# Kernel tuning notes

Measured on AMD Instinct MI355X. Metric: run time of the kernel, lower is better.

Reference implementation:

```python
import jax, jax.numpy as jnp
import numpy as np

DMODEL = 2048
HEADS = 16
DHEAD = DMODEL // HEADS  # 128


def setup_inputs() -> dict:
    key = jax.random.key(0)
    ks = jax.random.split(key, 9)
    s = 0.02
    x = jax.random.normal(ks[0], (4, 2048, DMODEL), dtype=jnp.float32)
    Wq = jax.random.normal(ks[1], (DMODEL, DMODEL), dtype=jnp.float32) * s
    bq = jax.random.normal(ks[2], (DMODEL,), dtype=jnp.float32) * s
    Wk = jax.random.normal(ks[3], (DMODEL, DMODEL), dtype=jnp.float32) * s
    bk = jax.random.normal(ks[4], (DMODEL,), dtype=jnp.float32) * s
    Wv = jax.random.normal(ks[5], (DMODEL, DMODEL), dtype=jnp.float32) * s
    bv = jax.random.normal(ks[6], (DMODEL,), dtype=jnp.float32) * s
    Wo = jax.random.normal(ks[7], (DMODEL, DMODEL), dtype=jnp.float32) * s
    bo = jax.random.normal(ks[8], (DMODEL,), dtype=jnp.float32) * s
    return {"x": x, "Wq": Wq, "bq": bq, "Wk": Wk, "bk": bk, "Wv": Wv, "bv": bv, "Wo": Wo, "bo": bo}


def reference(x, Wq, bq, Wk, bk, Wv, bv, Wo, bo):
    b, l, _ = x.shape
    # projections: [b, l, dmodel] -> [b, l, heads, dhead]
    q = (x @ Wq + bq).reshape(b, l, HEADS, DHEAD)
    k = (x @ Wk + bk).reshape(b, l, HEADS, DHEAD)
    v = (x @ Wv + bv).reshape(b, l, HEADS, DHEAD)
    # NOTE: source applies 1/sqrt(dhead) twice -> total scale 1/dhead (faithful)
    a = jnp.einsum('blhd,bLhd->bhlL', q, k) * (1.0 / DHEAD)
    a = jax.nn.softmax(a, axis=-1)
    prefinal = jnp.einsum('bhlL,bLhd->blhd', a, v)
    out = prefinal.reshape(b, l, HEADS * DHEAD) @ Wo + bo
    return out
```

## Files before the change

kernel.cpp:

```cpp
#include <hip/hip_runtime.h>

#define DMODEL 2048
#define SEQ    2048
#define BATCH  4
#define HEADS  16
#define DHEAD  128

typedef __attribute__((ext_vector_type(8))) short short8;
typedef __attribute__((ext_vector_type(4))) float f32x4;
typedef __attribute__((ext_vector_type(16))) float f32x16;

__device__ __forceinline__ unsigned short f2bf(float f) {
  union { float f; unsigned u; } v; v.f = f;
  unsigned r = v.u + 0x7FFFu + ((v.u >> 16) & 1u);
  return (unsigned short)(r >> 16);
}

__global__ __launch_bounds__(256) void cvt_f32_bf16(const float* __restrict__ in,
                                                    unsigned short* __restrict__ out,
                                                    int n4) {
  int i = blockIdx.x * 256 + threadIdx.x;
  if (i >= n4) return;
  float4 v = ((const float4*)in)[i];
  ushort4 o;
  o.x = f2bf(v.x); o.y = f2bf(v.y); o.z = f2bf(v.z); o.w = f2bf(v.w);
  ((ushort4*)out)[i] = o;
}

__global__ __launch_bounds__(256) void transpose_cvt4(const float* __restrict__ w0,
                                                      const float* __restrict__ w1,
                                                      const float* __restrict__ w2,
                                                      const float* __restrict__ w3,
                                                      unsigned short* __restrict__ o0,
                                                      unsigned short* __restrict__ o1,
                                                      unsigned short* __restrict__ o2,
                                                      unsigned short* __restrict__ o3) {
  __shared__ float tile[32][33];
  const int z = blockIdx.z;
  const float* in = (z == 0) ? w0 : (z == 1) ? w1 : (z == 2) ? w2 : w3;
  unsigned short* out = (z == 0) ? o0 : (z == 1) ? o1 : (z == 2) ? o2 : o3;
  const int tx = threadIdx.x, ty = threadIdx.y;
  const int x = blockIdx.x * 32 + tx;
  const int y0 = blockIdx.y * 32;
#pragma unroll
  for (int j = 0; j < 32; j += 8)
    tile[ty + j][tx] = in[(size_t)(y0 + ty + j) * DMODEL + x];
  __syncthreads();
  const int xo = blockIdx.y * 32 + tx;
  const int yo0 = blockIdx.x * 32;
#pragma unroll
  for (int j = 0; j < 32; j += 8)
    out[(size_t)(yo0 + ty + j) * DMODEL + xo] = f2bf(tile[tx][ty + j]);
}

__global__ __launch_bounds__(256) void transpose_v(const unsigned short* __restrict__ in,
                                                   unsigned short* __restrict__ out) {
  __shared__ unsigned short t[32][33];
  const int tx = threadIdx.x, ty = threadIdx.y;
  const int bid = blockIdx.x;
  const int lb = bid & 63;
  const int db = (bid >> 6) & 3;
  const int h  = (bid >> 8) & 15;
  const int b  = bid >> 12;
#pragma unroll
  for (int j = 0; j < 32; j += 8)
    t[ty + j][tx] = in[(size_t)(b * SEQ + lb * 32 + ty + j) * DMODEL + h * DHEAD + db * 32 + tx];
  __syncthreads();
  const size_t ob = ((size_t)(b * HEADS + h) * DHEAD + db * 32) * SEQ + lb * 32;
#pragma unroll
  for (int j = 0; j < 32; j += 8)
    out[ob + (size_t)(ty + j) * SEQ + tx] = t[tx][ty + j];
}

template <typename OUT_T, int NTN>
__global__ __launch_bounds__(512, 2) void gemm3(const unsigned short* __restrict__ A,
                                                const unsigned short* __restrict__ Bt,
                                                const float* __restrict__ b0,
                                                const float* __restrict__ b1,
                                                const float* __restrict__ b2,
                                                OUT_T* __restrict__ C) {
  __shared__ unsigned short As[2][256 * 32];
  __shared__ unsigned short Bs[2][256 * 32];

  const int tid = threadIdx.x;
  const int l = tid & 63, w = tid >> 6;
  const int wr = w >> 2, wc = w & 3;

  const int bid = blockIdx.x;
  int tm, tn;
  if constexpr (NTN == 24) {
    const int xcd = bid & 7;
    const int idx = bid >> 3;
    const int r = xcd >> 1, c = xcd & 1;
    const int mt = idx >> 4;
    const int i = idx & 15;
    const int mrow = mt & 1, mcol = mt >> 1;
    tm = r * 8 + mrow * 4 + (i & 3);
    tn = c * 12 + mcol * 4 + (i >> 2);
  } else {
    const int q8 = (32 * NTN) >> 3;
    const int swz = (bid & 7) * q8 + (bid >> 3);
    tn = swz % NTN;
    tm = swz / NTN;
  }

  const int srow = tid >> 2;
  const int schunk = (tid & 3) ^ ((tid >> 3) & 3);
  const unsigned short* Ag0 = A + (size_t)(tm * 256 + srow) * DMODEL + schunk * 8;
  const unsigned short* Ag1 = Ag0 + (size_t)128 * DMODEL;
  const unsigned short* Bg0 = Bt + (size_t)(tn * 256 + srow) * DMODEL + schunk * 8;
  const unsigned short* Bg1 = Bg0 + (size_t)128 * DMODEL;

#define GLL(src, dst) __builtin_amdgcn_global_load_lds( \
    (const __attribute__((address_space(1))) void*)(src), \
    (__attribute__((address_space(3))) void*)(dst), 16, 0, 0)

#define STAGE(bf, kt) do { \
    GLL(Ag0 + (kt) * 32, &As[bf][0 * 4096 + w * 512]); \
    GLL(Ag1 + (kt) * 32, &As[bf][1 * 4096 + w * 512]); \
    GLL(Bg0 + (kt) * 32, &Bs[bf][0 * 4096 + w * 512]); \
    GLL(Bg1 + (kt) * 32, &Bs[bf][1 * 4096 + w * 512]); \
  } while (0)

  f32x4 acc[8][4] = {};
  const int rchunk = ((l >> 4) ^ (((l & 15) >> 1) & 3)) * 8;

  STAGE(0, 0);
  int buf = 0;
  for (int t = 0; t < 64; ++t) {
    __builtin_amdgcn_s_barrier();
    __builtin_amdgcn_sched_barrier(0);
    if (t < 63) {
      STAGE(buf ^ 1, t + 1);
      __builtin_amdgcn_sched_barrier(0);
      asm volatile("s_waitcnt vmcnt(4)" ::: "memory");
    } else {
      asm volatile("s_waitcnt vmcnt(0)" ::: "memory");
    }
    __builtin_amdgcn_sched_barrier(0);
    __builtin_amdgcn_s_barrier();
    __builtin_amdgcn_sched_barrier(0);

    {
      const unsigned short* Asb = &As[buf][0];
      const unsigned short* Bsb = &Bs[buf][0];
      short8 bfr[4];
#pragma unroll
      for (int n = 0; n < 4; ++n) {
        const int row = wc * 64 + n * 16 + (l & 15);
        bfr[n] = *(const short8*)&Bsb[row * 32 + rchunk];
      }
      __builtin_amdgcn_s_setprio(1);
#pragma unroll
      for (int m = 0; m < 8; ++m) {
        const int row = wr * 128 + m * 16 + (l & 15);
        short8 af = *(const short8*)&Asb[row * 32 + rchunk];
#pragma unroll
        for (int n = 0; n < 4; ++n)
          acc[m][n] = __builtin_amdgcn_mfma_f32_16x16x32_bf16(af, bfr[n], acc[m][n], 0, 0, 0);
      }
      __builtin_amdgcn_s_setprio(0);
    }
    buf ^= 1;
  }
#undef STAGE
#undef GLL

  const int bsel = tn >> 3;
  const float* bp = (bsel == 0) ? b0 : ((bsel == 1) ? b1 : b2);
  OUT_T* Cb = C + (size_t)bsel * ((size_t)8192 * DMODEL);
  const int row0 = tm * 256 + wr * 128 + ((l >> 4) * 4);
  const int lc0 = (tn & 7) * 256 + wc * 64 + (l & 15);
#pragma unroll
  for (int n = 0; n < 4; ++n) {
    float bv = bp[lc0 + n * 16];
#pragma unroll
    for (int m = 0; m < 8; ++m) {
#pragma unroll
      for (int r = 0; r < 4; ++r) {
        float v = acc[m][n][r] + bv;
        size_t idx = (size_t)(row0 + m * 16 + r) * DMODEL + (lc0 + n * 16);
        if constexpr (sizeof(OUT_T) == 2) ((unsigned short*)Cb)[idx] = f2bf(v);
        else                              ((float*)Cb)[idx] = v;
      }
    }
  }
}

__global__ __launch_bounds__(256) void attn(const unsigned short* __restrict__ Q,
                                            const unsigned short* __restrict__ K,
                                            const unsigned short* __restrict__ V,
                                            unsigned short* __restrict__ O) {
  __shared__ unsigned short Ks[32 * 136];
  __shared__ unsigned short Vt[128 * 40];
  __shared__ unsigned short Ps[4][16 * 40];

  const int tid = threadIdx.x;
  const int l = tid & 63, w = tid >> 6;
  const int bh = blockIdx.x >> 5, qb = blockIdx.x & 31;
  const int b = bh >> 4, h = bh & 15;
  const size_t base = ((size_t)b * SEQ) * DMODEL + (size_t)h * DHEAD;

  const unsigned short* Qp = Q + base + (size_t)(qb * 64 + w * 16) * DMODEL;
  short8 qf[4];
#pragma unroll
  for (int dc = 0; dc < 4; ++dc)
    qf[dc] = *(const short8*)(Qp + (size_t)(l & 15) * DMODEL + dc * 32 + (l >> 4) * 8);

  f32x4 acc[8] = {};
  float sum[4] = {0.f, 0.f, 0.f, 0.f};

  const int skv = tid >> 3;
  const int sc = (tid & 7) * 16;
  const unsigned short* Kg = K + base + (size_t)skv * DMODEL + sc;
  const unsigned short* Vg = V + base + (size_t)skv * DMODEL + sc;

  const float cexp = 1.4426950408889634f / 128.0f;

  for (int kv0 = 0; kv0 < SEQ; kv0 += 32) {
    __syncthreads();
    short8 ka = *(const short8*)(Kg + (size_t)kv0 * DMODEL);
    short8 kb = *(const short8*)(Kg + (size_t)kv0 * DMODEL + 8);
    *(short8*)&Ks[skv * 136 + sc] = ka;
    *(short8*)&Ks[skv * 136 + sc + 8] = kb;
    short8 va = *(const short8*)(Vg + (size_t)kv0 * DMODEL);
    short8 vb = *(const short8*)(Vg + (size_t)kv0 * DMODEL + 8);
#pragma unroll
    for (int j = 0; j < 8; ++j) {
      Vt[(sc + j) * 40 + skv]     = (unsigned short)va[j];
      Vt[(sc + 8 + j) * 40 + skv] = (unsigned short)vb[j];
    }
    __syncthreads();

    f32x4 s[2];
#pragma unroll
    for (int nh = 0; nh < 2; ++nh) {
      f32x4 t = {};
#pragma unroll
      for (int dc = 0; dc < 4; ++dc) {
        short8 kf = *(const short8*)&Ks[(nh * 16 + (l & 15)) * 136 + dc * 32 + (l >> 4) * 8];
        t = __builtin_amdgcn_mfma_f32_16x16x32_bf16(qf[dc], kf, t, 0, 0, 0);
      }
      s[nh] = t;
    }

#pragma unroll
    for (int nh = 0; nh < 2; ++nh) {
#pragma unroll
      for (int r = 0; r < 4; ++r) {
        float p = exp2f(s[nh][r] * cexp);
        sum[r] += p;
        Ps[w][((l >> 4) * 4 + r) * 40 + (l & 15) + nh * 16] = f2bf(p);
      }
    }

    short8 pf = *(const short8*)&Ps[w][(l & 15) * 40 + (l >> 4) * 8];
#pragma unroll
    for (int db = 0; db < 8; ++db) {
      short8 vf = *(const short8*)&Vt[(db * 16 + (l & 15)) * 40 + (l >> 4) * 8];
      acc[db] = __builtin_amdgcn_mfma_f32_16x16x32_bf16(pf, vf, acc[db], 0, 0, 0);
    }
  }

  float inv[4];
#pragma unroll
  for (int r = 0; r < 4; ++r) {
    float s = sum[r];
    s += __shfl_xor(s, 1);
    s += __shfl_xor(s, 2);
    s += __shfl_xor(s, 4);
    s += __shfl_xor(s, 8);
    inv[r] = 1.0f / s;
  }
  unsigned short* Op = O + base + (size_t)(qb * 64 + w * 16) * DMODEL;
#pragma unroll
  for (int db = 0; db < 8; ++db)
#pragma unroll
    for (int r = 0; r < 4; ++r)
      Op[(size_t)((l >> 4) * 4 + r) * DMODEL + db * 16 + (l & 15)] = f2bf(acc[db][r] * inv[r]);
}

__global__ __launch_bounds__(256, 2) void attn6(const unsigned short* __restrict__ Q,
                                                const unsigned short* __restrict__ K,
                                                const unsigned short* __restrict__ VT,
                                                unsigned short* __restrict__ O) {
  __shared__ unsigned short Ks[2][64 * 128];
  __shared__ unsigned short Vs[2][128 * 64];

  const int tid = threadIdx.x;
  const int l = tid & 63, w = tid >> 6;
  const int x32 = l & 31, h = l >> 5;

  const int bid = blockIdx.x;
  const int swz = (bid & 7) * 64 + (bid >> 3);
  const int bh = swz >> 3, qb = swz & 7;
  const int b = bh >> 4, hh = bh & 15;
  const size_t base = ((size_t)b * SEQ) * DMODEL + (size_t)hh * DHEAD;
  const unsigned short* VTb = VT + (size_t)bh * DHEAD * SEQ;

  const unsigned short* Qp = Q + base + (size_t)(qb * 256 + w * 64) * DMODEL;
  short8 qfA[8], qfB[8];
#pragma unroll
  for (int dc = 0; dc < 8; ++dc) {
    qfA[dc] = *(const short8*)(Qp + (size_t)x32 * DMODEL + dc * 16 + h * 8);
    qfB[dc] = *(const short8*)(Qp + (size_t)(x32 + 32) * DMODEL + dc * 16 + h * 8);
  }

  const unsigned short* Kg0 = K + base + (size_t)(w * 16 + (l >> 4)) * DMODEL + (((l & 15) ^ (l >> 4)) * 8);
  const unsigned short* Kg1 = K + base + (size_t)(w * 16 + (l >> 4)) * DMODEL + (((l & 15) ^ ((l >> 4) + 4)) * 8);
  const unsigned short* Vg0 = VTb + (size_t)(w * 32 + (l >> 3)) * SEQ + (((l & 7) ^ (l >> 3)) * 8);

  unsigned short* KsD = &Ks[0][0];
  unsigned short* VsD = &Vs[0][0];

#define GLL(src, dst) __builtin_amdgcn_global_load_lds( \
    (const __attribute__((address_space(1))) void*)(src), \
    (__attribute__((address_space(3))) void*)(dst), 16, 0, 0)

#define STAGE(bf, kv0) do { \
    GLL(Kg0 + (size_t)(kv0) * DMODEL,        KsD + (bf) * 8192 + w * 2048 + 0 * 512); \
    GLL(Kg1 + (size_t)((kv0) + 4) * DMODEL,  KsD + (bf) * 8192 + w * 2048 + 1 * 512); \
    GLL(Kg0 + (size_t)((kv0) + 8) * DMODEL,  KsD + (bf) * 8192 + w * 2048 + 2 * 512); \
    GLL(Kg1 + (size_t)((kv0) + 12) * DMODEL, KsD + (bf) * 8192 + w * 2048 + 3 * 512); \
    GLL(Vg0 + (size_t)0 * SEQ + (kv0),       VsD + (bf) * 8192 + w * 2048 + 0 * 512); \
    GLL(Vg0 + (size_t)8 * SEQ + (kv0),       VsD + (bf) * 8192 + w * 2048 + 1 * 512); \
    GLL(Vg0 + (size_t)16 * SEQ + (kv0),      VsD + (bf) * 8192 + w * 2048 + 2 * 512); \
    GLL(Vg0 + (size_t)24 * SEQ + (kv0),      VsD + (bf) * 8192 + w * 2048 + 3 * 512); \
  } while (0)

  f32x16 acc0[4] = {}, acc1[4] = {};
  float sum0 = 0.f, sum1 = 0.f;
  const float cexp = 1.4426950408889634f / 128.0f;

#define COMPUTE_SUB(bf, s) do { \
    const unsigned short* Kb_ = &Ks[bf][(s) * 32 * 128]; \
    const unsigned short* Vb_ = &Vs[bf][0]; \
    f32x16 sa0 = {}, sa1 = {}; \
    __builtin_amdgcn_s_setprio(1); \
    _Pragma("unroll") \
    for (int dc = 0; dc < 8; ++dc) { \
      short8 kf = *(const short8*)&Kb_[x32 * 128 + (((dc * 2 + h) ^ (x32 & 7)) * 8)]; \
      sa0 = __builtin_amdgcn_mfma_f32_32x32x16_bf16(kf, qfA[dc], sa0, 0, 0, 0); \
      sa1 = __builtin_amdgcn_mfma_f32_32x32x16_bf16(kf, qfB[dc], sa1, 0, 0, 0); \
    } \
    __builtin_amdgcn_s_setprio(0); \
    union { unsigned u[4]; short8 s8; } pf0A, pf1A, pf0B, pf1B; \
    { \
      float p[16]; \
      _Pragma("unroll") \
      for (int r = 0; r < 16; ++r) { p[r] = __builtin_amdgcn_exp2f(sa0[r] * cexp); sum0 += p[r]; } \
      unsigned pk0[4], pk1[4]; \
      _Pragma("unroll") \
      for (int blk = 0; blk < 4; ++blk) { \
        asm("v_cvt_pk_bf16_f32 %0, %1, %2" : "=v"(pk0[blk]) : "v"(p[blk * 4 + 0]), "v"(p[blk * 4 + 1])); \
        asm("v_cvt_pk_bf16_f32 %0, %1, %2" : "=v"(pk1[blk]) : "v"(p[blk * 4 + 2]), "v"(p[blk * 4 + 3])); \
      } \
      unsigned a0 = pk0[0], a1 = pk0[1], b0 = pk1[0], b1 = pk1[1]; \
      asm("v_permlane32_swap_b32 %0, %1" : "+v"(a0), "+v"(a1)); \
      asm("v_permlane32_swap_b32 %0, %1" : "+v"(b0), "+v"(b1)); \
      pf0A.u[0] = a0; pf0A.u[1] = b0; pf0A.u[2] = a1; pf0A.u[3] = b1; \
      unsigned c0 = pk0[2], c1 = pk0[3], d0 = pk1[2], d1 = pk1[3]; \
      asm("v_permlane32_swap_b32 %0, %1" : "+v"(c0), "+v"(c1)); \
      asm("v_permlane32_swap_b32 %0, %1" : "+v"(d0), "+v"(d1)); \
      pf1A.u[0] = c0; pf1A.u[1] = d0; pf1A.u[2] = c1; pf1A.u[3] = d1; \
    } \
    { \
      float p[16]; \
      _Pragma("unroll") \
      for (int r = 0; r < 16; ++r) { p[r] = __builtin_amdgcn_exp2f(sa1[r] * cexp); sum1 += p[r]; } \
      unsigned pk0[4], pk1[4]; \
      _Pragma("unroll") \
      for (int blk = 0; blk < 4; ++blk) { \
        asm("v_cvt_pk_bf16_f32 %0, %1, %2" : "=v"(pk0[blk]) : "v"(p[blk * 4 + 0]), "v"(p[blk * 4 + 1])); \
        asm("v_cvt_pk_bf16_f32 %0, %1, %2" : "=v"(pk1[blk]) : "v"(p[blk * 4 + 2]), "v"(p[blk * 4 + 3])); \
      } \
      unsigned a0 = pk0[0], a1 = pk0[1], b0 = pk1[0], b1 = pk1[1]; \
      asm("v_permlane32_swap_b32 %0, %1" : "+v"(a0), "+v"(a1)); \
      asm("v_permlane32_swap_b32 %0, %1" : "+v"(b0), "+v"(b1)); \
      pf0B.u[0] = a0; pf0B.u[1] = b0; pf0B.u[2] = a1; pf0B.u[3] = b1; \
      unsigned c0 = pk0[2], c1 = pk0[3], d0 = pk1[2], d1 = pk1[3]; \
      asm("v_permlane32_swap_b32 %0, %1" : "+v"(c0), "+v"(c1)); \
      asm("v_permlane32_swap_b32 %0, %1" : "+v"(d0), "+v"(d1)); \
      pf1B.u[0] = c0; pf1B.u[1] = d0; pf1B.u[2] = c1; pf1B.u[3] = d1; \
    } \
    __builtin_amdgcn_s_setprio(1); \
    _Pragma("unroll") \
    for (int db = 0; db < 4; ++db) { \
      const int row = db * 32 + x32; \
      short8 vf0 = *(const short8*)&Vb_[row * 64 + ((((s) * 4 + 0 + h) ^ (row & 7)) * 8)]; \
      short8 vf1 = *(const short8*)&Vb_[row * 64 + ((((s) * 4 + 2 + h) ^ (row & 7)) * 8)]; \
      acc0[db] = __builtin_amdgcn_mfma_f32_32x32x16_bf16(pf0A.s8, vf0, acc0[db], 0, 0, 0); \
      acc1[db] = __builtin_amdgcn_mfma_f32_32x32x16_bf16(pf0B.s8, vf0, acc1[db], 0, 0, 0); \
      acc0[db] = __builtin_amdgcn_mfma_f32_32x32x16_bf16(pf1A.s8, vf1, acc0[db], 0, 0, 0); \
      acc1[db] = __builtin_amdgcn_mfma_f32_32x32x16_bf16(pf1B.s8, vf1, acc1[db], 0, 0, 0); \
    } \
    __builtin_amdgcn_s_setprio(0); \
  } while (0)

  STAGE(0, 0);
  int buf = 0;
  for (int t = 0; t < 32; ++t) {
    __builtin_amdgcn_s_barrier();
    __builtin_amdgcn_sched_barrier(0);
    if (t < 31) {
      STAGE(buf ^ 1, (t + 1) * 64);
      __builtin_amdgcn_sched_barrier(0);
      asm volatile("s_waitcnt vmcnt(8)" ::: "memory");
    } else {
      asm volatile("s_waitcnt vmcnt(0)" ::: "memory");
    }
    __builtin_amdgcn_sched_barrier(0);
    __builtin_amdgcn_s_barrier();
    __builtin_amdgcn_sched_barrier(0);
    COMPUTE_SUB(buf, 0);
    COMPUTE_SUB(buf, 1);
    buf ^= 1;
  }
#undef COMPUTE_SUB
#undef STAGE
#undef GLL

  sum0 += __shfl_xor(sum0, 32);
  sum1 += __shfl_xor(sum1, 32);
  float inv0 = 1.0f / sum0;
  float inv1 = 1.0f / sum1;
  float invq0[16], invq1[16];
#pragma unroll
  for (int r = 0; r < 16; ++r) {
    const int crow = (r & 3) + 8 * (r >> 2) + 4 * h;
    invq0[r] = __shfl(inv0, crow);
    invq1[r] = __shfl(inv1, crow);
  }

  unsigned short* Op = O + base + (size_t)(qb * 256 + w * 64) * DMODEL;
#pragma unroll
  for (int db = 0; db < 4; ++db)
#pragma unroll
    for (int r = 0; r < 16; ++r) {
      const int crow = (r & 3) + 8 * (r >> 2) + 4 * h;
      Op[(size_t)crow * DMODEL + db * 32 + x32] = f2bf(acc0[db][r] * invq0[r]);
      Op[(size_t)(crow + 32) * DMODEL + db * 32 + x32] = f2bf(acc1[db][r] * invq1[r]);
    }
}

extern "C" void kernel_launch(void* const* d_in, const int* in_sizes, int n_in,
                              void* d_out, int out_size, void* d_ws, size_t ws_size,
                              hipStream_t stream) {
  const float* x  = (const float*)d_in[0];
  const float* Wq = (const float*)d_in[1];
  const float* bq = (const float*)d_in[2];
  const float* Wk = (const float*)d_in[3];
  const float* bk = (const float*)d_in[4];
  const float* Wv = (const float*)d_in[5];
  const float* bv = (const float*)d_in[6];
  const float* Wo = (const float*)d_in[7];
  const float* bo = (const float*)d_in[8];

  char* ws = (char*)d_ws;
  unsigned short* xb  = (unsigned short*)ws;
  unsigned short* WqT = (unsigned short*)(ws + 33554432);
  unsigned short* WkT = (unsigned short*)(ws + 41943040);
  unsigned short* WvT = (unsigned short*)(ws + 50331648);
  unsigned short* WoT = (unsigned short*)(ws + 58720256);
  unsigned short* Qb  = (unsigned short*)(ws + 67108864);
  unsigned short* Kb  = (unsigned short*)(ws + 100663296);
  unsigned short* Vb  = (unsigned short*)(ws + 134217728);
  unsigned short* VTg = (unsigned short*)(ws + 167772160);
  unsigned short* Pf  = xb;

  const bool vt_ok = (ws_size >= (size_t)201326592);

  cvt_f32_bf16<<<16384, 256, 0, stream>>>(x, xb, (BATCH * SEQ * DMODEL) / 4);

  transpose_cvt4<<<dim3(64, 64, 4), dim3(32, 8), 0, stream>>>(Wq, Wk, Wv, Wo, WqT, WkT, WvT, WoT);

  gemm3<unsigned short, 24><<<768, 512, 0, stream>>>(xb, WqT, bq, bk, bv, Qb);

  if (vt_ok) {
    transpose_v<<<16384, dim3(32, 8), 0, stream>>>(Vb, VTg);
    attn6<<<512, 256, 0, stream>>>(Qb, Kb, VTg, Pf);
  } else {
    attn<<<2048, 256, 0, stream>>>(Qb, Kb, Vb, Pf);
  }

  gemm3<float, 8><<<256, 512, 0, stream>>>(Pf, WoT, bo, bo, bo, (float*)d_out);
}
```

Baseline: 580.8 us.

## Restructure projection GEMM to 4 waves with 128x128 warp tiles and K=64 stages

Replaces the 8-wave, 256x256-tile GEMM (64x128 per-wave sub-tiles, K-step 32) with a 4-wave version where each wave computes a 128x128 sub-tile and each LDS stage covers K=64 with an XOR swizzle over 8 chunks. This raises MFMA work per LDS fragment load and halves the number of barrier-synchronised iterations. In exchange the 256 accumulator registers per lane push the kernel to one block per CU, and LDS use doubles to 128 KB, which cuts occupancy and latency hiding.

```diff
diff --git a/kernel.cpp b/kernel.cpp
--- a/kernel.cpp
+++ b/kernel.cpp
@@ -73,18 +73,18 @@
 }
 
 template <typename OUT_T, int NTN>
-__global__ __launch_bounds__(512, 2) void gemm3(const unsigned short* __restrict__ A,
+__global__ __launch_bounds__(256, 1) void gemm6(const unsigned short* __restrict__ A,
                                                 const unsigned short* __restrict__ Bt,
                                                 const float* __restrict__ b0,
                                                 const float* __restrict__ b1,
                                                 const float* __restrict__ b2,
                                                 OUT_T* __restrict__ C) {
-  __shared__ unsigned short As[2][256 * 32];
-  __shared__ unsigned short Bs[2][256 * 32];
+  __shared__ unsigned short As[2][256 * 64];
+  __shared__ unsigned short Bs[2][256 * 64];
 
   const int tid = threadIdx.x;
   const int l = tid & 63, w = tid >> 6;
-  const int wr = w >> 2, wc = w & 3;
+  const int wr = w >> 1, wc = w & 1;
 
   const int bid = blockIdx.x;
   int tm, tn;
@@ -104,36 +104,45 @@
     tm = swz / NTN;
   }
 
-  const int srow = tid >> 2;
-  const int schunk = (tid & 3) ^ ((tid >> 3) & 3);
-  const unsigned short* Ag0 = A + (size_t)(tm * 256 + srow) * DMODEL + schunk * 8;
-  const unsigned short* Ag1 = Ag0 + (size_t)128 * DMODEL;
-  const unsigned short* Bg0 = Bt + (size_t)(tn * 256 + srow) * DMODEL + schunk * 8;
-  const unsigned short* Bg1 = Bg0 + (size_t)128 * DMODEL;
+  const int srow = tid >> 3;
+  const int schunk = (tid & 7) ^ ((tid >> 3) & 7);
+  const unsigned short* Ag = A + (size_t)(tm * 256 + srow) * DMODEL + schunk * 8;
+  const unsigned short* Bg = Bt + (size_t)(tn * 256 + srow) * DMODEL + schunk * 8;
 
 #define GLL(src, dst) __builtin_amdgcn_global_load_lds( \
     (const __attribute__((address_space(1))) void*)(src), \
     (__attribute__((address_space(3))) void*)(dst), 16, 0, 0)
 
 #define STAGE(bf, kt) do { \
-    GLL(Ag0 + (kt) * 32, &As[bf][0 * 4096 + w * 512]); \
-    GLL(Ag1 + (kt) * 32, &As[bf][1 * 4096 + w * 512]); \
-    GLL(Bg0 + (kt) * 32, &Bs[bf][0 * 4096 + w * 512]); \
-    GLL(Bg1 + (kt) * 32, &Bs[bf][1 * 4096 + w * 512]); \
+    GLL(Ag + (size_t)(0 * 32) * DMODEL + (kt) * 64, &As[bf][0 * 2048 + w * 512]); \
+    GLL(Ag + (size_t)(1 * 32) * DMODEL + (kt) * 64, &As[bf][1 * 2048 + w * 512]); \
+    GLL(Ag + (size_t)(2 * 32) * DMODEL + (kt) * 64, &As[bf][2 * 2048 + w * 512]); \
+    GLL(Ag + (size_t)(3 * 32) * DMODEL + (kt) * 64, &As[bf][3 * 2048 + w * 512]); \
+    GLL(Ag + (size_t)(4 * 32) * DMODEL + (kt) * 64, &As[bf][4 * 2048 + w * 512]); \
+    GLL(Ag + (size_t)(5 * 32) * DMODEL + (kt) * 64, &As[bf][5 * 2048 + w * 512]); \
+    GLL(Ag + (size_t)(6 * 32) * DMODEL + (kt) * 64, &As[bf][6 * 2048 + w * 512]); \
+    GLL(Ag + (size_t)(7 * 32) * DMODEL + (kt) * 64, &As[bf][7 * 2048 + w * 512]); \
+    GLL(Bg + (size_t)(0 * 32) * DMODEL + (kt) * 64, &Bs[bf][0 * 2048 + w * 512]); \
+    GLL(Bg + (size_t)(1 * 32) * DMODEL + (kt) * 64, &Bs[bf][1 * 2048 + w * 512]); \
+    GLL(Bg + (size_t)(2 * 32) * DMODEL + (kt) * 64, &Bs[bf][2 * 2048 + w * 512]); \
+    GLL(Bg + (size_t)(3 * 32) * DMODEL + (kt) * 64, &Bs[bf][3 * 2048 + w * 512]); \
+    GLL(Bg + (size_t)(4 * 32) * DMODEL + (kt) * 64, &Bs[bf][4 * 2048 + w * 512]); \
+    GLL(Bg + (size_t)(5 * 32) * DMODEL + (kt) * 64, &Bs[bf][5 * 2048 + w * 512]); \
+    GLL(Bg + (size_t)(6 * 32) * DMODEL + (kt) * 64, &Bs[bf][6 * 2048 + w * 512]); \
+    GLL(Bg + (size_t)(7 * 32) * DMODEL + (kt) * 64, &Bs[bf][7 * 2048 + w * 512]); \
   } while (0)
 
-  f32x4 acc[8][4] = {};
-  const int rchunk = ((l >> 4) ^ (((l & 15) >> 1) & 3)) * 8;
+  f32x4 acc[8][8] = {};
 
   STAGE(0, 0);
   int buf = 0;
-  for (int t = 0; t < 64; ++t) {
+  for (int t = 0; t < 32; ++t) {
     __builtin_amdgcn_s_barrier();
     __builtin_amdgcn_sched_barrier(0);
-    if (t < 63) {
+    if (t < 31) {
       STAGE(buf ^ 1, t + 1);
       __builtin_amdgcn_sched_barrier(0);
-      asm volatile("s_waitcnt vmcnt(4)" ::: "memory");
+      asm volatile("s_waitcnt vmcnt(16)" ::: "memory");
     } else {
       asm volatile("s_waitcnt vmcnt(0)" ::: "memory");
     }
@@ -144,20 +153,25 @@
     {
       const unsigned short* Asb = &As[buf][0];
       const unsigned short* Bsb = &Bs[buf][0];
-      short8 bfr[4];
-#pragma unroll
-      for (int n = 0; n < 4; ++n) {
-        const int row = wc * 64 + n * 16 + (l & 15);
-        bfr[n] = *(const short8*)&Bsb[row * 32 + rchunk];
+      short8 bfr[8][2];
+#pragma unroll
+      for (int n = 0; n < 8; ++n) {
+        const int row = wc * 128 + n * 16 + (l & 15);
+#pragma unroll
+        for (int ks = 0; ks < 2; ++ks)
+          bfr[n][ks] = *(const short8*)&Bsb[row * 64 + (((ks * 4 + (l >> 4)) ^ (row & 7)) * 8)];
       }
       __builtin_amdgcn_s_setprio(1);
 #pragma unroll
       for (int m = 0; m < 8; ++m) {
         const int row = wr * 128 + m * 16 + (l & 15);
-        short8 af = *(const short8*)&Asb[row * 32 + rchunk];
-#pragma unroll
-        for (int n = 0; n < 4; ++n)
-          acc[m][n] = __builtin_amdgcn_mfma_f32_16x16x32_bf16(af, bfr[n], acc[m][n], 0, 0, 0);
+        short8 af0 = *(const short8*)&Asb[row * 64 + (((0 + (l >> 4)) ^ (row & 7)) * 8)];
+        short8 af1 = *(const short8*)&Asb[row * 64 + (((4 + (l >> 4)) ^ (row & 7)) * 8)];
+#pragma unroll
+        for (int n = 0; n < 8; ++n) {
+          acc[m][n] = __builtin_amdgcn_mfma_f32_16x16x32_bf16(af0, bfr[n][0], acc[m][n], 0, 0, 0);
+          acc[m][n] = __builtin_amdgcn_mfma_f32_16x16x32_bf16(af1, bfr[n][1], acc[m][n], 0, 0, 0);
+        }
       }
       __builtin_amdgcn_s_setprio(0);
     }
@@ -170,9 +184,9 @@
   const float* bp = (bsel == 0) ? b0 : ((bsel == 1) ? b1 : b2);
   OUT_T* Cb = C + (size_t)bsel * ((size_t)8192 * DMODEL);
   const int row0 = tm * 256 + wr * 128 + ((l >> 4) * 4);
-  const int lc0 = (tn & 7) * 256 + wc * 64 + (l & 15);
-#pragma unroll
-  for (int n = 0; n < 4; ++n) {
+  const int lc0 = (tn & 7) * 256 + wc * 128 + (l & 15);
+#pragma unroll
+  for (int n = 0; n < 8; ++n) {
     float bv = bp[lc0 + n * 16];
 #pragma unroll
     for (int m = 0; m < 8; ++m) {
@@ -474,7 +488,7 @@
 
   transpose_cvt4<<<dim3(64, 64, 4), dim3(32, 8), 0, stream>>>(Wq, Wk, Wv, Wo, WqT, WkT, WvT, WoT);
 
-  gemm3<unsigned short, 24><<<768, 512, 0, stream>>>(xb, WqT, bq, bk, bv, Qb);
+  gemm6<unsigned short, 24><<<768, 256, 0, stream>>>(xb, WqT, bq, bk, bv, Qb);
 
   if (vt_ok) {
     transpose_v<<<16384, dim3(32, 8), 0, stream>>>(Vb, VTg);
@@ -483,5 +497,5 @@
     attn<<<2048, 256, 0, stream>>>(Qb, Kb, Vb, Pf);
   }
 
-  gemm3<float, 8><<<256, 512, 0, stream>>>(Pf, WoT, bo, bo, bo, (float*)d_out);
-}
+  gemm6<float, 8><<<256, 256, 0, stream>>>(Pf, WoT, bo, bo, bo, (float*)d_out);
+}
```

Result: faster. 549.6 us (-5.4%).
